# Optimization experiments

Measured on AMD Instinct MI355X. Metric: run time of the kernel, lower is better.

Reference implementation:

```python
import jax, jax.numpy as jnp
import numpy as np

EPS = 1e-12  # matches torch F.normalize clamp_min eps
SCALE = 20.0
NEG = -1e9


def l2norm(x):
    return x / jnp.maximum(jnp.linalg.norm(x, axis=-1, keepdims=True), EPS)


def setup_inputs() -> dict:
    key = jax.random.key(0)
    B, P, A, DV, DT, E = 32, 192, 30, 768, 768, 256
    ks = jax.random.split(key, 8)
    visual_feature = jax.random.normal(ks[0], (B, 1 + P, DV), jnp.float32)
    textual_feature = jax.random.normal(ks[1], (B, 1 + A, DT), jnp.float32)
    att_nums = jax.random.randint(ks[2], (B,), 1, A + 1)  # valid attr counts >=1
    # mask==1 marks padded attribute slots (consistent with att_nums)
    mask = (jnp.arange(A)[None, :] >= att_nums[:, None]).astype(jnp.int32)
    W_vis = 0.02 * jax.random.normal(ks[3], (E, DV), jnp.float32)
    W_txt = 0.02 * jax.random.normal(ks[4], (E, DT), jnp.float32)
    W_patch = 0.02 * jax.random.normal(ks[5], (E, DV), jnp.float32)
    W_att = 0.02 * jax.random.normal(ks[6], (E, DT), jnp.float32)
    z = jnp.zeros((E,), jnp.float32)
    return {
        "visual_feature": visual_feature, "textual_feature": textual_feature,
        "mask": mask, "att_nums": att_nums,
        "W_vis": W_vis, "b_vis": z, "W_txt": W_txt, "b_txt": z,
        "W_patch": W_patch, "b_patch": z, "W_att": W_att, "b_att": z,
    }


def reference(visual_feature, textual_feature, mask, att_nums,
              W_vis, b_vis, W_txt, b_txt, W_patch, b_patch, W_att, b_att):
    # token splits + linear projections
    visual_embed = visual_feature[:, 0] @ W_vis.T + b_vis        # [Bv, E]
    patch = visual_feature[:, 1:] @ W_patch.T + b_patch           # [Bv, P, E]
    textual_embed = textual_feature[:, 0] @ W_txt.T + b_txt       # [Bt, E]
    att = textual_feature[:, 1:] @ W_att.T + b_att                # [Bt, A, E]

    pad = mask.astype(bool)                                       # [Bt, A], True = padded

    # attention 1: each text's attributes attend over every image's patches
    s1 = jax.nn.relu(jnp.einsum('tae,vpe->vtap', l2norm(att), l2norm(patch))) * SCALE
    attn1 = jax.nn.softmax(s1, axis=-1)                           # [Bv, Bt, A, P]
    attend_patch = jnp.einsum('vtap,vpe->vtae', attn1, patch)     # [Bv, Bt, A, E]
    attend_patch = jnp.where(pad[None, :, :, None], 0.0, attend_patch)

    # attention 2: each image's patches attend over every text's attributes (masked)
    s2 = jax.nn.relu(jnp.einsum('vpe,tae->tvpa', l2norm(patch), l2norm(att))) * SCALE
    s2 = jnp.where(pad[:, None, None, :], NEG, s2)                # [Bt, Bv, P, A]
    attn2 = jax.nn.softmax(s2, axis=-1)
    attend_att = jnp.einsum('tvpa,tae->tvpe', attn2, att)         # [Bt, Bv, P, E]

    # local similarity
    ap = l2norm(attend_patch)                                     # [Bv, Bt, A, E]
    aa = l2norm(attend_att)                                       # [Bt, Bv, P, E]
    an = att_nums.astype(aa.dtype)
    sim = jnp.einsum('tvpe,vtae->tvpa', aa, ap) / an[:, None, None, None]
    local_similarity = sim.sum(axis=2).mean(axis=2)               # [Bt, Bv]

    # training-path global embeds
    patch_mean = patch.mean(axis=1)                               # [Bv, E]
    att_mean = (att / an[:, None, None]).sum(axis=1)              # [Bt, E]

    return (visual_embed, textual_embed, patch_mean, att_mean, local_similarity)
```

## Files before the change

kernel.cpp:

```cpp
#include <hip/hip_runtime.h>
#include <math.h>

#define D_IN 768
#define E_DIM 256
#define NB 32
#define NP 192
#define NA 30

#define A_SLOTS (452 * 24 * 64)
#define B_SLOTS (4 * 16 * 24 * 64)

typedef __attribute__((ext_vector_type(8))) __bf16 bf16x8;
typedef __attribute__((ext_vector_type(4))) float f32x4;

__device__ __forceinline__ bf16x8 cvt8(float4 a, float4 b) {
    bf16x8 v;
    v[0]=(__bf16)a.x; v[1]=(__bf16)a.y; v[2]=(__bf16)a.z; v[3]=(__bf16)a.w;
    v[4]=(__bf16)b.x; v[5]=(__bf16)b.y; v[6]=(__bf16)b.z; v[7]=(__bf16)b.w;
    return v;
}

__global__ __launch_bounds__(256) void prepack_kernel(
    const float* __restrict__ vf, const float* __restrict__ tf,
    const float* __restrict__ Wp, const float* __restrict__ Wa,
    const float* __restrict__ Wv, const float* __restrict__ Wt,
    __bf16* __restrict__ Apack, __bf16* __restrict__ Bpack)
{
    const int s = blockIdx.x * 256 + threadIdx.x;
    if (s < A_SLOTS) {
        const int r16 = s / 1536;
        const int rem = s - r16 * 1536;
        const int kt = rem >> 6, l = rem & 63;
        const int row16 = l & 15;
        const int k0 = kt * 32 + (l >> 4) * 8;
        const float* src;
        if (r16 < 384) {
            const int v = r16 / 12, sub = r16 - 12 * v;
            src = vf + (size_t)(v * 193 + 1 + sub * 16 + row16) * D_IN;
        } else if (r16 < 448) {
            const int u = r16 - 384, t = u >> 1, half = u & 1;
            const int ridx = half * 16 + row16;
            const int r = (ridx < NA) ? ridx : 0;
            src = tf + (size_t)(t * 31 + 1 + r) * D_IN;
        } else if (r16 < 450) {
            src = vf + (size_t)((r16 - 448) * 16 + row16) * 193 * D_IN;
        } else {
            src = tf + (size_t)((r16 - 450) * 16 + row16) * 31 * D_IN;
        }
        float4 f0 = *(const float4*)&src[k0];
        float4 f1 = *(const float4*)&src[k0 + 4];
        *(bf16x8*)&Apack[(size_t)s * 8] = cvt8(f0, f1);
    } else {
        const int u = s - A_SLOTS;
        const int mat = u / 24576;
        const int rem = u - mat * 24576;
        const int ntile = rem / 1536;
        const int rem2 = rem - ntile * 1536;
        const int kt = rem2 >> 6, l = rem2 & 63;
        const float* W;
        if (mat == 0)      W = Wp;
        else if (mat == 1) W = Wa;
        else if (mat == 2) W = Wv;
        else               W = Wt;
        const int k0 = kt * 32 + (l >> 4) * 8;
        const float* src = W + (size_t)(ntile * 16 + (l & 15)) * D_IN;
        float4 f0 = *(const float4*)&src[k0];
        float4 f1 = *(const float4*)&src[k0 + 4];
        *(bf16x8*)&Bpack[(size_t)u * 8] = cvt8(f0, f1);
    }
}

__global__ __launch_bounds__(256) void gemm_frag_kernel(
    const __bf16* __restrict__ Apack, const __bf16* __restrict__ Bpack,
    __bf16* __restrict__ Ybf)
{
    const int bid = blockIdx.x;
    const int r16 = bid >> 2, cg = bid & 3;
    const int tid = threadIdx.x;
    const int w = tid >> 6, l = tid & 63, q = l >> 4, n15 = l & 15;
    const int ntg = cg * 4 + w;
    const int mat = (r16 < 384) ? 0 : (r16 < 448) ? 1 : (r16 < 450) ? 2 : 3;

    const __bf16* Ab = Apack + (size_t)r16 * 24 * 512 + l * 8;
    const __bf16* Bb = Bpack + (size_t)(mat * 16 + ntg) * 24 * 512 + l * 8;

    f32x4 acc = {0.f, 0.f, 0.f, 0.f};
    #pragma unroll 8
    for (int kt = 0; kt < 24; ++kt) {
        bf16x8 a = *(const bf16x8*)&Ab[kt * 512];
        bf16x8 b = *(const bf16x8*)&Bb[kt * 512];
        acc = __builtin_amdgcn_mfma_f32_16x16x32_bf16(a, b, acc, 0, 0, 0);
    }

    const int col = ntg * 16 + n15;
    #pragma unroll
    for (int r = 0; r < 4; ++r)
        Ybf[(size_t)(r16 * 16 + q * 4 + r) * E_DIM + col] = (__bf16)acc[r];
}

__global__ __launch_bounds__(256) void pack_kernel(
    const __bf16* __restrict__ Ybf,
    const float* __restrict__ bv, const float* __restrict__ bt,
    const float* __restrict__ bp, const float* __restrict__ ba,
    const int* __restrict__ att_nums,
    float* __restrict__ out_vis, float* __restrict__ out_txt,
    float* __restrict__ out_pm, float* __restrict__ out_am,
    __bf16* __restrict__ pn_frag, __bf16* __restrict__ pB_frag,
    __bf16* __restrict__ an_frag, __bf16* __restrict__ attT_frag)
{
    __shared__ float LDSf[32 * 260];
    __shared__ float invn_s[32];

    const int bid = blockIdx.x;
    const int tid = threadIdx.x;

    int role, base;
    const float* bias;
    if (bid < 192)       { role = 0; base = 32 * bid;              bias = bp; }
    else if (bid < 224)  { role = 1; base = 6144 + 32 * (bid-192); bias = ba; }
    else if (bid == 224) { role = 2; base = 7168;                  bias = bv; }
    else                 { role = 3; base = 7200;                  bias = bt; }

    if (role >= 2) {
        float* outp = (role == 2) ? out_vis : out_txt;
        const float b = bias[tid];
        #pragma unroll
        for (int i = 0; i < 32; ++i)
            outp[i * E_DIM + tid] = (float)Ybf[(size_t)(base + i) * E_DIM + tid] + b;
        return;
    }

    {
        const float b = bias[tid];
        #pragma unroll
        for (int i = 0; i < 32; ++i)
            LDSf[i * 260 + tid] = (float)Ybf[(size_t)(base + i) * E_DIM + tid] + b;
    }
    __syncthreads();

    if (role == 0) {
        const int v = bid / 6, c = bid - 6 * v;
        {
            const int row = tid >> 3, seg = tid & 7;
            const float* rr = &LDSf[row * 260 + seg * 32];
            float ssq = 0.f;
            #pragma unroll
            for (int j = 0; j < 32; ++j) ssq += rr[j] * rr[j];
            ssq += __shfl_xor(ssq, 1, 64);
            ssq += __shfl_xor(ssq, 2, 64);
            ssq += __shfl_xor(ssq, 4, 64);
            if (seg == 0) invn_s[row] = 1.f / fmaxf(sqrtf(ssq), 1e-12f);
        }
        {
            float s = 0.f;
            #pragma unroll
            for (int r = 0; r < 32; ++r) s += LDSf[r * 260 + tid];
            atomicAdd(&out_pm[v * E_DIM + tid], s * (1.f / 192.f));
        }
        __syncthreads();
        __bf16* dstn = pn_frag + (size_t)(v * 6 + c) * 8192;
        #pragma unroll
        for (int i = 0; i < 4; ++i) {
            const int slot = tid + 256 * i;
            const int mt = slot >> 9, koct = (slot >> 6) & 7, lane = slot & 63;
            const int prl = mt * 16 + (lane & 15);
            const int e0 = koct * 32 + (lane >> 4) * 8;
            const float inr = invn_s[prl];
            const float* src = &LDSf[prl * 260 + e0];
            bf16x8 vv;
            #pragma unroll
            for (int j = 0; j < 8; ++j) vv[j] = (__bf16)(src[j] * inr);
            *(bf16x8*)&dstn[slot * 8] = vv;
        }
        __bf16* dstb = pB_frag + (size_t)(v * 6 + c) * 8192;
        #pragma unroll
        for (int i = 0; i < 4; ++i) {
            const int slot = tid + 256 * i;
            const int nt = slot >> 6, lane = slot & 63;
            const int e = nt * 16 + (lane & 15);
            const int p0 = (lane >> 4) * 8;
            bf16x8 vv;
            #pragma unroll
            for (int j = 0; j < 8; ++j) vv[j] = (__bf16)LDSf[(p0 + j) * 260 + e];
            *(bf16x8*)&dstb[slot * 8] = vv;
        }
    } else {
        const int t = bid - 192;
        const int Av = att_nums[t];
        {
            const int row = tid >> 3, seg = tid & 7;
            const float* rr = &LDSf[row * 260 + seg * 32];
            float ssq = 0.f;
            #pragma unroll
            for (int j = 0; j < 32; ++j) ssq += rr[j] * rr[j];
            ssq += __shfl_xor(ssq, 1, 64);
            ssq += __shfl_xor(ssq, 2, 64);
            ssq += __shfl_xor(ssq, 4, 64);
            if (seg == 0) invn_s[row] = (row < NA) ? 1.f / fmaxf(sqrtf(ssq), 1e-12f) : 0.f;
        }
        {
            float s = 0.f;
            #pragma unroll
            for (int r = 0; r < NA; ++r) s += LDSf[r * 260 + tid];
            out_am[t * E_DIM + tid] = s / (float)Av;
        }
        __syncthreads();
        __bf16* dstn = an_frag + (size_t)t * 8192;
        #pragma unroll
        for (int i = 0; i < 4; ++i) {
            const int slot = tid + 256 * i;
            const int at = slot >> 9, koct = (slot >> 6) & 7, lane = slot & 63;
            const int a = at * 16 + (lane & 15);
            const int e0 = koct * 32 + (lane >> 4) * 8;
            const float inr = (a < NA) ? invn_s[a] : 0.f;
            const float* src = &LDSf[a * 260 + e0];
            bf16x8 vv;
            #pragma unroll
            for (int j = 0; j < 8; ++j) vv[j] = (__bf16)(src[j] * inr);
            *(bf16x8*)&dstn[slot * 8] = vv;
        }
        __bf16* dstb = attT_frag + (size_t)t * 8192;
        #pragma unroll
        for (int i = 0; i < 4; ++i) {
            const int slot = tid + 256 * i;
            const int nt = slot >> 6, lane = slot & 63;
            const int e = nt * 16 + (lane & 15);
            const int a0 = (lane >> 4) * 8;
            bf16x8 vv;
            #pragma unroll
            for (int j = 0; j < 8; ++j)
                vv[j] = (a0 + j < NA) ? (__bf16)LDSf[(a0 + j) * 260 + e] : (__bf16)0.f;
            *(bf16x8*)&dstb[slot * 8] = vv;
        }
    }
}

__global__ __launch_bounds__(256) void pair_mfma_kernel(
    const __bf16* __restrict__ pn_frag, const __bf16* __restrict__ pB_frag,
    const __bf16* __restrict__ an_frag, const __bf16* __restrict__ attT_frag,
    const int* __restrict__ att_nums, float* __restrict__ out_sim)
{
    __shared__ __align__(16) __bf16 an_s[8192];
    __shared__ __align__(16) __bf16 attT_s[8192];
    __shared__ __align__(16) __bf16 pn_s[8192];
    __shared__ __align__(16) __bf16 pB_s[8192];
    __shared__ __align__(16) __bf16 Xa_s[1024];
    __shared__ __align__(16) __bf16 XaT_s[1024];
    __shared__ float red_s[128];
    __shared__ float invn_s[32];
    __shared__ float wred_s[4];

    const int v = blockIdx.x, t = blockIdx.y;
    const int tid = threadIdx.x;
    const int w = tid >> 6, l = tid & 63, q = l >> 4, n15 = l & 15;
    const int Av = att_nums[t];

    {
        const __bf16* s1 = an_frag + (size_t)t * 8192;
        const __bf16* s2 = attT_frag + (size_t)t * 8192;
        #pragma unroll
        for (int i = 0; i < 4; ++i) {
            const int slot = tid + 256 * i;
            *(bf16x8*)&an_s[slot * 8]   = *(const bf16x8*)&s1[slot * 8];
            *(bf16x8*)&attT_s[slot * 8] = *(const bf16x8*)&s2[slot * 8];
        }
    }
    __syncthreads();

    bf16x8 ab[4];
    #pragma unroll
    for (int n = 0; n < 4; ++n)
        ab[n] = *(const bf16x8*)&attT_s[((w * 4 + n) * 64 + l) * 8];

    f32x4 apacc[2][4];
    #pragma unroll
    for (int m = 0; m < 2; ++m)
        #pragma unroll
        for (int n = 0; n < 4; ++n) { f32x4 z = {0.f,0.f,0.f,0.f}; apacc[m][n] = z; }
    float sa_acc[4] = {0.f, 0.f, 0.f, 0.f};

    for (int c = 0; c < 6; ++c) {
        __syncthreads();
        {
            const __bf16* sp1 = pn_frag + (size_t)(v * 6 + c) * 8192;
            const __bf16* sp2 = pB_frag + (size_t)(v * 6 + c) * 8192;
            #pragma unroll
            for (int i = 0; i < 4; ++i) {
                const int slot = tid + 256 * i;
                *(bf16x8*)&pn_s[slot * 8] = *(const bf16x8*)&sp1[slot * 8];
                *(bf16x8*)&pB_s[slot * 8] = *(const bf16x8*)&sp2[slot * 8];
            }
        }
        __syncthreads();

        {
            const int mt = w >> 1, at = w & 1;
            f32x4 sacc = {0.f, 0.f, 0.f, 0.f};
            #pragma unroll
            for (int kp = 0; kp < 8; ++kp) {
                bf16x8 af  = *(const bf16x8*)&pn_s[((mt * 8 + kp) * 64 + l) * 8];
                bf16x8 bf_ = *(const bf16x8*)&an_s[((at * 8 + kp) * 64 + l) * 8];
                sacc = __builtin_amdgcn_mfma_f32_16x16x32_bf16(af, bf_, sacc, 0, 0, 0);
            }
            const int a = at * 16 + n15;
            #pragma unroll
            for (int r = 0; r < 4; ++r) {
                const int pcl = q * 4 + r;
                const int pcc = mt * 16 + pcl;
                float xvv = (a < Av) ? __expf(fmaxf(20.f * sacc[r], 0.f)) : 0.f;
                __bf16 h = (__bf16)xvv;
                Xa_s[mt * 512 + (pcl + 16 * (a >> 3)) * 8 + (a & 7)] = h;
                XaT_s[at * 512 + (n15 + 16 * (pcc >> 3)) * 8 + (pcc & 7)] = h;
            }
        }
        __syncthreads();

        f32x4 aacc[2][4];
        {
            bf16x8 xa0 = *(const bf16x8*)&Xa_s[l * 8];
            bf16x8 xa1 = *(const bf16x8*)&Xa_s[512 + l * 8];
            bf16x8 xt0 = *(const bf16x8*)&XaT_s[l * 8];
            bf16x8 xt1 = *(const bf16x8*)&XaT_s[512 + l * 8];
            #pragma unroll
            for (int n = 0; n < 4; ++n) {
                f32x4 z = {0.f, 0.f, 0.f, 0.f};
                aacc[0][n] = __builtin_amdgcn_mfma_f32_16x16x32_bf16(xa0, ab[n], z, 0, 0, 0);
                aacc[1][n] = __builtin_amdgcn_mfma_f32_16x16x32_bf16(xa1, ab[n], z, 0, 0, 0);
                bf16x8 pb = *(const bf16x8*)&pB_s[((w * 4 + n) * 64 + l) * 8];
                apacc[0][n] = __builtin_amdgcn_mfma_f32_16x16x32_bf16(xt0, pb, apacc[0][n], 0, 0, 0);
                apacc[1][n] = __builtin_amdgcn_mfma_f32_16x16x32_bf16(xt1, pb, apacc[1][n], 0, 0, 0);
            }
        }

        #pragma unroll
        for (int mt2 = 0; mt2 < 2; ++mt2)
            #pragma unroll
            for (int r = 0; r < 4; ++r) {
                float ssq = 0.f;
                #pragma unroll
                for (int n = 0; n < 4; ++n) { float vv = aacc[mt2][n][r]; ssq += vv * vv; }
                ssq += __shfl_xor(ssq, 1, 64);
                ssq += __shfl_xor(ssq, 2, 64);
                ssq += __shfl_xor(ssq, 4, 64);
                ssq += __shfl_xor(ssq, 8, 64);
                if (n15 == 0) red_s[(mt2 * 16 + q * 4 + r) * 4 + w] = ssq;
            }
        __syncthreads();
        if (tid < 32) {
            float s = red_s[tid * 4] + red_s[tid * 4 + 1] + red_s[tid * 4 + 2] + red_s[tid * 4 + 3];
            invn_s[tid] = 1.f / fmaxf(sqrtf(s), 1e-12f);
        }
        __syncthreads();
        #pragma unroll
        for (int mt2 = 0; mt2 < 2; ++mt2)
            #pragma unroll
            for (int r = 0; r < 4; ++r) {
                const float inr = invn_s[mt2 * 16 + q * 4 + r];
                #pragma unroll
                for (int n = 0; n < 4; ++n) sa_acc[n] += aacc[mt2][n][r] * inr;
            }
    }

    #pragma unroll
    for (int mt2 = 0; mt2 < 2; ++mt2)
        #pragma unroll
        for (int r = 0; r < 4; ++r) {
            float ssq = 0.f;
            #pragma unroll
            for (int n = 0; n < 4; ++n) { float vv = apacc[mt2][n][r]; ssq += vv * vv; }
            ssq += __shfl_xor(ssq, 1, 64);
            ssq += __shfl_xor(ssq, 2, 64);
            ssq += __shfl_xor(ssq, 4, 64);
            ssq += __shfl_xor(ssq, 8, 64);
            if (n15 == 0) red_s[(mt2 * 16 + q * 4 + r) * 4 + w] = ssq;
        }
    __syncthreads();
    if (tid < 32) {
        float s = red_s[tid * 4] + red_s[tid * 4 + 1] + red_s[tid * 4 + 2] + red_s[tid * 4 + 3];
        invn_s[tid] = 1.f / fmaxf(sqrtf(s), 1e-12f);
    }
    __syncthreads();

    float prod = 0.f;
    #pragma unroll
    for (int n = 0; n < 4; ++n) {
        float sp = 0.f;
        #pragma unroll
        for (int mt2 = 0; mt2 < 2; ++mt2)
            #pragma unroll
            for (int r = 0; r < 4; ++r)
                sp += apacc[mt2][n][r] * invn_s[mt2 * 16 + q * 4 + r];
        float saf = sa_acc[n];
        saf += __shfl_xor(saf, 16, 64);
        saf += __shfl_xor(saf, 32, 64);
        float spf = sp;
        spf += __shfl_xor(spf, 16, 64);
        spf += __shfl_xor(spf, 32, 64);
        prod += saf * spf;
    }
    prod += __shfl_xor(prod, 1, 64);
    prod += __shfl_xor(prod, 2, 64);
    prod += __shfl_xor(prod, 4, 64);
    prod += __shfl_xor(prod, 8, 64);
    prod += __shfl_xor(prod, 16, 64);
    prod += __shfl_xor(prod, 32, 64);
    if (l == 0) wred_s[w] = prod;
    __syncthreads();
    if (tid == 0)
        out_sim[t * NB + v] = (wred_s[0] + wred_s[1] + wred_s[2] + wred_s[3]) * 0.25f
                              / ((float)Av * 30.f);
}

extern "C" void kernel_launch(void* const* d_in, const int* in_sizes, int n_in,
                              void* d_out, int out_size, void* d_ws, size_t ws_size,
                              hipStream_t stream)
{
    const float* vf = (const float*)d_in[0];
    const float* tf = (const float*)d_in[1];
    const int*   an = (const int*)d_in[3];
    const float* Wv = (const float*)d_in[4];
    const float* bv = (const float*)d_in[5];
    const float* Wt = (const float*)d_in[6];
    const float* bt = (const float*)d_in[7];
    const float* Wp = (const float*)d_in[8];
    const float* bp = (const float*)d_in[9];
    const float* Wa = (const float*)d_in[10];
    const float* ba = (const float*)d_in[11];

    float* out = (float*)d_out;
    float* out_vis = out;
    float* out_txt = out + 8192;
    float* out_pm  = out + 16384;
    float* out_am  = out + 24576;
    float* out_sim = out + 32768;

    __bf16* Ybf = (__bf16*)d_ws;
    char* region2 = (char*)d_ws + 3702784;
    __bf16* Apack = (__bf16*)region2;
    __bf16* Bpack = Apack + (size_t)A_SLOTS * 8;
    __bf16* pn_frag   = (__bf16*)region2;
    __bf16* pB_frag   = pn_frag + 1572864;
    __bf16* an_frag   = pn_frag + 3145728;
    __bf16* attT_frag = pn_frag + 3407872;

    hipMemsetAsync((char*)d_out + 16384 * sizeof(float), 0, 8192 * sizeof(float), stream);

    prepack_kernel<<<(A_SLOTS + B_SLOTS) / 256, 256, 0, stream>>>(
        vf, tf, Wp, Wa, Wv, Wt, Apack, Bpack);

    gemm_frag_kernel<<<452 * 4, 256, 0, stream>>>(Apack, Bpack, Ybf);

    pack_kernel<<<226, 256, 0, stream>>>(
        Ybf, bv, bt, bp, ba, an,
        out_vis, out_txt, out_pm, out_am,
        pn_frag, pB_frag, an_frag, attT_frag);

    pair_mfma_kernel<<<dim3(NB, NB), 256, 0, stream>>>(
        pn_frag, pB_frag, an_frag, attT_frag, an, out_sim);
}
```

Before: 154.7 us.

## Fuse projection GEMM with fragment packing and stream pair-kernel operands from global

Merges the projection GEMM and the pack/normalize kernel into one kernel where each block computes a 16-row strip across all 256 columns, keeping results in LDS instead of round-tripping through a bf16 Ybf buffer. The output-zeroing memset is folded into the prepack kernel, and att_mean now accumulates via atomics from two half-blocks. In the pair kernel, patch and attribute fragments are read directly from global into registers rather than staged through LDS, and the norm reduction is recomputed per lane to remove barriers. This cuts launches, intermediate traffic and LDS usage, but the fused GEMM has fewer blocks (452) and the pair kernel now depends on cache hits for repeated global fragment loads.

```diff
diff --git a/kernel.cpp b/kernel.cpp
--- a/kernel.cpp
+++ b/kernel.cpp
@@ -24,9 +24,11 @@
     const float* __restrict__ vf, const float* __restrict__ tf,
     const float* __restrict__ Wp, const float* __restrict__ Wa,
     const float* __restrict__ Wv, const float* __restrict__ Wt,
-    __bf16* __restrict__ Apack, __bf16* __restrict__ Bpack)
+    __bf16* __restrict__ Apack, __bf16* __restrict__ Bpack,
+    float* __restrict__ out_zero)
 {
     const int s = blockIdx.x * 256 + threadIdx.x;
+    if (s < 16384) out_zero[s] = 0.f;
     if (s < A_SLOTS) {
         const int r16 = s / 1536;
         const int rem = s - r16 * 1536;
@@ -70,36 +72,8 @@
     }
 }
 
-__global__ __launch_bounds__(256) void gemm_frag_kernel(
+__global__ __launch_bounds__(256) void gemm_pack_kernel(
     const __bf16* __restrict__ Apack, const __bf16* __restrict__ Bpack,
-    __bf16* __restrict__ Ybf)
-{
-    const int bid = blockIdx.x;
-    const int r16 = bid >> 2, cg = bid & 3;
-    const int tid = threadIdx.x;
-    const int w = tid >> 6, l = tid & 63, q = l >> 4, n15 = l & 15;
-    const int ntg = cg * 4 + w;
-    const int mat = (r16 < 384) ? 0 : (r16 < 448) ? 1 : (r16 < 450) ? 2 : 3;
-
-    const __bf16* Ab = Apack + (size_t)r16 * 24 * 512 + l * 8;
-    const __bf16* Bb = Bpack + (size_t)(mat * 16 + ntg) * 24 * 512 + l * 8;
-
-    f32x4 acc = {0.f, 0.f, 0.f, 0.f};
-    #pragma unroll 8
-    for (int kt = 0; kt < 24; ++kt) {
-        bf16x8 a = *(const bf16x8*)&Ab[kt * 512];
-        bf16x8 b = *(const bf16x8*)&Bb[kt * 512];
-        acc = __builtin_amdgcn_mfma_f32_16x16x32_bf16(a, b, acc, 0, 0, 0);
-    }
-
-    const int col = ntg * 16 + n15;
-    #pragma unroll
-    for (int r = 0; r < 4; ++r)
-        Ybf[(size_t)(r16 * 16 + q * 4 + r) * E_DIM + col] = (__bf16)acc[r];
-}
-
-__global__ __launch_bounds__(256) void pack_kernel(
-    const __bf16* __restrict__ Ybf,
     const float* __restrict__ bv, const float* __restrict__ bt,
     const float* __restrict__ bp, const float* __restrict__ ba,
     const int* __restrict__ att_nums,
@@ -108,169 +82,152 @@
     __bf16* __restrict__ pn_frag, __bf16* __restrict__ pB_frag,
     __bf16* __restrict__ an_frag, __bf16* __restrict__ attT_frag)
 {
-    __shared__ float LDSf[32 * 260];
-    __shared__ float invn_s[32];
-
-    const int bid = blockIdx.x;
+    __shared__ float LDSf[16 * 260];
+    __shared__ float invn_s[16];
+
+    const int r16 = blockIdx.x;
     const int tid = threadIdx.x;
-
-    int role, base;
-    const float* bias;
-    if (bid < 192)       { role = 0; base = 32 * bid;              bias = bp; }
-    else if (bid < 224)  { role = 1; base = 6144 + 32 * (bid-192); bias = ba; }
-    else if (bid == 224) { role = 2; base = 7168;                  bias = bv; }
-    else                 { role = 3; base = 7200;                  bias = bt; }
-
-    if (role >= 2) {
-        float* outp = (role == 2) ? out_vis : out_txt;
-        const float b = bias[tid];
-        #pragma unroll
-        for (int i = 0; i < 32; ++i)
-            outp[i * E_DIM + tid] = (float)Ybf[(size_t)(base + i) * E_DIM + tid] + b;
+    const int w = tid >> 6, l = tid & 63, q = l >> 4, n15 = l & 15;
+    const int mat = (r16 < 384) ? 0 : (r16 < 448) ? 1 : (r16 < 450) ? 2 : 3;
+    const float* bias = (mat == 0) ? bp : (mat == 1) ? ba : (mat == 2) ? bv : bt;
+
+    const __bf16* Ab = Apack + (size_t)r16 * 24 * 512 + l * 8;
+    const __bf16* Bb = Bpack + ((size_t)(mat * 16 + w * 4) * 24 * 512) + l * 8;
+
+    f32x4 acc[4];
+    #pragma unroll
+    for (int n = 0; n < 4; ++n) { f32x4 z = {0.f,0.f,0.f,0.f}; acc[n] = z; }
+
+    #pragma unroll 6
+    for (int kt = 0; kt < 24; ++kt) {
+        bf16x8 a = *(const bf16x8*)&Ab[kt * 512];
+        #pragma unroll
+        for (int nt = 0; nt < 4; ++nt) {
+            bf16x8 b = *(const bf16x8*)&Bb[(size_t)nt * 24 * 512 + kt * 512];
+            acc[nt] = __builtin_amdgcn_mfma_f32_16x16x32_bf16(a, b, acc[nt], 0, 0, 0);
+        }
+    }
+
+    #pragma unroll
+    for (int nt = 0; nt < 4; ++nt) {
+        const int col = w * 64 + nt * 16 + n15;
+        const float b = bias[col];
+        #pragma unroll
+        for (int r = 0; r < 4; ++r)
+            LDSf[(q * 4 + r) * 260 + col] = acc[nt][r] + b;
+    }
+    __syncthreads();
+
+    if (mat >= 2) {
+        float* outp = (mat == 2) ? out_vis : out_txt;
+        const int rowbase = (mat == 2) ? (r16 - 448) * 16 : (r16 - 450) * 16;
+        #pragma unroll
+        for (int i = 0; i < 16; ++i)
+            outp[(rowbase + i) * E_DIM + tid] = LDSf[i * 260 + tid];
         return;
     }
 
+    const bool is_patch = (mat == 0);
+    int vc = 0, mt = 0, t = 0, Av = 1;
+    if (is_patch) {
+        const int v = r16 / 12, sub = r16 - 12 * v;
+        vc = v * 6 + (sub >> 1);  mt = sub & 1;
+    } else {
+        const int u = r16 - 384;
+        t = u >> 1;  mt = u & 1;  Av = att_nums[t];
+    }
+
     {
-        const float b = bias[tid];
-        #pragma unroll
-        for (int i = 0; i < 32; ++i)
-            LDSf[i * 260 + tid] = (float)Ybf[(size_t)(base + i) * E_DIM + tid] + b;
-    }
-    __syncthreads();
-
-    if (role == 0) {
-        const int v = bid / 6, c = bid - 6 * v;
-        {
-            const int row = tid >> 3, seg = tid & 7;
-            const float* rr = &LDSf[row * 260 + seg * 32];
-            float ssq = 0.f;
-            #pragma unroll
-            for (int j = 0; j < 32; ++j) ssq += rr[j] * rr[j];
-            ssq += __shfl_xor(ssq, 1, 64);
-            ssq += __shfl_xor(ssq, 2, 64);
-            ssq += __shfl_xor(ssq, 4, 64);
-            if (seg == 0) invn_s[row] = 1.f / fmaxf(sqrtf(ssq), 1e-12f);
-        }
-        {
-            float s = 0.f;
-            #pragma unroll
-            for (int r = 0; r < 32; ++r) s += LDSf[r * 260 + tid];
-            atomicAdd(&out_pm[v * E_DIM + tid], s * (1.f / 192.f));
-        }
-        __syncthreads();
-        __bf16* dstn = pn_frag + (size_t)(v * 6 + c) * 8192;
-        #pragma unroll
-        for (int i = 0; i < 4; ++i) {
-            const int slot = tid + 256 * i;
-            const int mt = slot >> 9, koct = (slot >> 6) & 7, lane = slot & 63;
-            const int prl = mt * 16 + (lane & 15);
+        const int row = tid >> 4, seg = tid & 15;
+        const float* rr = &LDSf[row * 260 + seg * 16];
+        float ssq = 0.f;
+        #pragma unroll
+        for (int j = 0; j < 16; ++j) ssq += rr[j] * rr[j];
+        ssq += __shfl_xor(ssq, 1, 64);
+        ssq += __shfl_xor(ssq, 2, 64);
+        ssq += __shfl_xor(ssq, 4, 64);
+        ssq += __shfl_xor(ssq, 8, 64);
+        if (seg == 0) {
+            const bool valid = is_patch || (mt * 16 + row < NA);
+            invn_s[row] = valid ? 1.f / fmaxf(sqrtf(ssq), 1e-12f) : 0.f;
+        }
+    }
+    {
+        const int nrows = is_patch ? 16 : (mt == 0 ? 16 : 14);
+        float s = 0.f;
+        for (int r = 0; r < nrows; ++r) s += LDSf[r * 260 + tid];
+        if (is_patch) atomicAdd(&out_pm[(r16 / 12) * E_DIM + tid], s * (1.f / 192.f));
+        else          atomicAdd(&out_am[t * E_DIM + tid], s / (float)Av);
+    }
+    __syncthreads();
+
+    {
+        __bf16* dstn = (is_patch ? pn_frag + (size_t)vc * 8192
+                                 : an_frag + (size_t)t * 8192) + (size_t)mt * 4096;
+        #pragma unroll
+        for (int ii = 0; ii < 2; ++ii) {
+            const int s2 = tid + 256 * ii;
+            const int koct = s2 >> 6, lane = s2 & 63;
+            const int rloc = lane & 15;
             const int e0 = koct * 32 + (lane >> 4) * 8;
-            const float inr = invn_s[prl];
-            const float* src = &LDSf[prl * 260 + e0];
+            const float inr = invn_s[rloc];
+            const float* src = &LDSf[rloc * 260 + e0];
             bf16x8 vv;
             #pragma unroll
             for (int j = 0; j < 8; ++j) vv[j] = (__bf16)(src[j] * inr);
-            *(bf16x8*)&dstn[slot * 8] = vv;
-        }
-        __bf16* dstb = pB_frag + (size_t)(v * 6 + c) * 8192;
-        #pragma unroll
-        for (int i = 0; i < 4; ++i) {
-            const int slot = tid + 256 * i;
-            const int nt = slot >> 6, lane = slot & 63;
-            const int e = nt * 16 + (lane & 15);
-            const int p0 = (lane >> 4) * 8;
+            *(bf16x8*)&dstn[(size_t)s2 * 8] = vv;
+        }
+    }
+    {
+        __bf16* dstb = is_patch ? pB_frag + (size_t)vc * 8192
+                                : attT_frag + (size_t)t * 8192;
+        #pragma unroll
+        for (int ii = 0; ii < 2; ++ii) {
+            const int s2 = tid + 256 * ii;
+            const int nt = s2 >> 5, li = s2 & 31;
+            const int lane = 32 * mt + li;
+            const int p0 = (li >> 4) * 8;
+            const int e = nt * 16 + (li & 15);
             bf16x8 vv;
             #pragma unroll
-            for (int j = 0; j < 8; ++j) vv[j] = (__bf16)LDSf[(p0 + j) * 260 + e];
-            *(bf16x8*)&dstb[slot * 8] = vv;
-        }
-    } else {
-        const int t = bid - 192;
-        const int Av = att_nums[t];
-        {
-            const int row = tid >> 3, seg = tid & 7;
-            const float* rr = &LDSf[row * 260 + seg * 32];
-            float ssq = 0.f;
-            #pragma unroll
-            for (int j = 0; j < 32; ++j) ssq += rr[j] * rr[j];
-            ssq += __shfl_xor(ssq, 1, 64);
-            ssq += __shfl_xor(ssq, 2, 64);
-            ssq += __shfl_xor(ssq, 4, 64);
-            if (seg == 0) invn_s[row] = (row < NA) ? 1.f / fmaxf(sqrtf(ssq), 1e-12f) : 0.f;
-        }
-        {
-            float s = 0.f;
-            #pragma unroll
-            for (int r = 0; r < NA; ++r) s += LDSf[r * 260 + tid];
-            out_am[t * E_DIM + tid] = s / (float)Av;
-        }
-        __syncthreads();
-        __bf16* dstn = an_frag + (size_t)t * 8192;
-        #pragma unroll
-        for (int i = 0; i < 4; ++i) {
-            const int slot = tid + 256 * i;
-            const int at = slot >> 9, koct = (slot >> 6) & 7, lane = slot & 63;
-            const int a = at * 16 + (lane & 15);
-            const int e0 = koct * 32 + (lane >> 4) * 8;
-            const float inr = (a < NA) ? invn_s[a] : 0.f;
-            const float* src = &LDSf[a * 260 + e0];
-            bf16x8 vv;
-            #pragma unroll
-            for (int j = 0; j < 8; ++j) vv[j] = (__bf16)(src[j] * inr);
-            *(bf16x8*)&dstn[slot * 8] = vv;
-        }
-        __bf16* dstb = attT_frag + (size_t)t * 8192;
-        #pragma unroll
-        for (int i = 0; i < 4; ++i) {
-            const int slot = tid + 256 * i;
-            const int nt = slot >> 6, lane = slot & 63;
-            const int e = nt * 16 + (lane & 15);
-            const int a0 = (lane >> 4) * 8;
-            bf16x8 vv;
-            #pragma unroll
-            for (int j = 0; j < 8; ++j)
-                vv[j] = (a0 + j < NA) ? (__bf16)LDSf[(a0 + j) * 260 + e] : (__bf16)0.f;
-            *(bf16x8*)&dstb[slot * 8] = vv;
+            for (int j = 0; j < 8; ++j) {
+                float val = LDSf[(p0 + j) * 260 + e];
+                if (!is_patch && (mt * 16 + p0 + j >= NA)) val = 0.f;
+                vv[j] = (__bf16)val;
+            }
+            *(bf16x8*)&dstb[(size_t)(nt * 64 + lane) * 8] = vv;
         }
     }
 }
 
-__global__ __launch_bounds__(256) void pair_mfma_kernel(
+__global__ __launch_bounds__(256, 3) void pair_mfma_kernel(
     const __bf16* __restrict__ pn_frag, const __bf16* __restrict__ pB_frag,
     const __bf16* __restrict__ an_frag, const __bf16* __restrict__ attT_frag,
     const int* __restrict__ att_nums, float* __restrict__ out_sim)
 {
     __shared__ __align__(16) __bf16 an_s[8192];
-    __shared__ __align__(16) __bf16 attT_s[8192];
-    __shared__ __align__(16) __bf16 pn_s[8192];
-    __shared__ __align__(16) __bf16 pB_s[8192];
     __shared__ __align__(16) __bf16 Xa_s[1024];
     __shared__ __align__(16) __bf16 XaT_s[1024];
     __shared__ float red_s[128];
-    __shared__ float invn_s[32];
     __shared__ float wred_s[4];
 
     const int v = blockIdx.x, t = blockIdx.y;
     const int tid = threadIdx.x;
     const int w = tid >> 6, l = tid & 63, q = l >> 4, n15 = l & 15;
     const int Av = att_nums[t];
+    const int mt = w >> 1, at = w & 1;
 
     {
         const __bf16* s1 = an_frag + (size_t)t * 8192;
-        const __bf16* s2 = attT_frag + (size_t)t * 8192;
         #pragma unroll
         for (int i = 0; i < 4; ++i) {
             const int slot = tid + 256 * i;
-            *(bf16x8*)&an_s[slot * 8]   = *(const bf16x8*)&s1[slot * 8];
-            *(bf16x8*)&attT_s[slot * 8] = *(const bf16x8*)&s2[slot * 8];
-        }
-    }
-    __syncthreads();
-
-    bf16x8 ab[4];
-    #pragma unroll
-    for (int n = 0; n < 4; ++n)
-        ab[n] = *(const bf16x8*)&attT_s[((w * 4 + n) * 64 + l) * 8];
+            *(bf16x8*)&an_s[slot * 8] = *(const bf16x8*)&s1[slot * 8];
+        }
+    }
+    __syncthreads();
+
+    const __bf16* atb = attT_frag + (size_t)t * 8192;
 
     f32x4 apacc[2][4];
     #pragma unroll
@@ -280,25 +237,21 @@
     float sa_acc[4] = {0.f, 0.f, 0.f, 0.f};
 
     for (int c = 0; c < 6; ++c) {
-        __syncthreads();
+        const __bf16* pnb = pn_frag + (size_t)(v * 6 + c) * 8192;
+        const __bf16* pbb = pB_frag + (size_t)(v * 6 + c) * 8192;
+
+        bf16x8 pb[4], ab[4];
+        #pragma unroll
+        for (int n = 0; n < 4; ++n) {
+            pb[n] = *(const bf16x8*)&pbb[((w * 4 + n) * 64 + l) * 8];
+            ab[n] = *(const bf16x8*)&atb[((w * 4 + n) * 64 + l) * 8];
+        }
+
         {
-            const __bf16* sp1 = pn_frag + (size_t)(v * 6 + c) * 8192;
-            const __bf16* sp2 = pB_frag + (size_t)(v * 6 + c) * 8192;
-            #pragma unroll
-            for (int i = 0; i < 4; ++i) {
-                const int slot = tid + 256 * i;
-                *(bf16x8*)&pn_s[slot * 8] = *(const bf16x8*)&sp1[slot * 8];
-                *(bf16x8*)&pB_s[slot * 8] = *(const bf16x8*)&sp2[slot * 8];
-            }
-        }
-        __syncthreads();
-
-        {
-            const int mt = w >> 1, at = w & 1;
             f32x4 sacc = {0.f, 0.f, 0.f, 0.f};
             #pragma unroll
             for (int kp = 0; kp < 8; ++kp) {
-                bf16x8 af  = *(const bf16x8*)&pn_s[((mt * 8 + kp) * 64 + l) * 8];
+                bf16x8 af  = *(const bf16x8*)&pnb[((mt * 8 + kp) * 64 + l) * 8];
                 bf16x8 bf_ = *(const bf16x8*)&an_s[((at * 8 + kp) * 64 + l) * 8];
                 sacc = __builtin_amdgcn_mfma_f32_16x16x32_bf16(af, bf_, sacc, 0, 0, 0);
             }
@@ -326,12 +279,10 @@
                 f32x4 z = {0.f, 0.f, 0.f, 0.f};
                 aacc[0][n] = __builtin_amdgcn_mfma_f32_16x16x32_bf16(xa0, ab[n], z, 0, 0, 0);
                 aacc[1][n] = __builtin_amdgcn_mfma_f32_16x16x32_bf16(xa1, ab[n], z, 0, 0, 0);
-                bf16x8 pb = *(const bf16x8*)&pB_s[((w * 4 + n) * 64 + l) * 8];
-                apacc[0][n] = __builtin_amdgcn_mfma_f32_16x16x32_bf16(xt0, pb, apacc[0][n], 0, 0, 0);
-                apacc[1][n] = __builtin_amdgcn_mfma_f32_16x16x32_bf16(xt1, pb, apacc[1][n], 0, 0, 0);
-            }
-        }
-
+                apacc[0][n] = __builtin_amdgcn_mfma_f32_16x16x32_bf16(xt0, pb[n], apacc[0][n], 0, 0, 0);
+                apacc[1][n] = __builtin_amdgcn_mfma_f32_16x16x32_bf16(xt1, pb[n], apacc[1][n], 0, 0, 0);
+            }
+        }
         #pragma unroll
         for (int mt2 = 0; mt2 < 2; ++mt2)
             #pragma unroll
@@ -346,21 +297,20 @@
                 if (n15 == 0) red_s[(mt2 * 16 + q * 4 + r) * 4 + w] = ssq;
             }
         __syncthreads();
-        if (tid < 32) {
-            float s = red_s[tid * 4] + red_s[tid * 4 + 1] + red_s[tid * 4 + 2] + red_s[tid * 4 + 3];
-            invn_s[tid] = 1.f / fmaxf(sqrtf(s), 1e-12f);
-        }
-        __syncthreads();
         #pragma unroll
         for (int mt2 = 0; mt2 < 2; ++mt2)
             #pragma unroll
             for (int r = 0; r < 4; ++r) {
-                const float inr = invn_s[mt2 * 16 + q * 4 + r];
+                const int row = mt2 * 16 + q * 4 + r;
+                const float s = red_s[row * 4] + red_s[row * 4 + 1]
+                              + red_s[row * 4 + 2] + red_s[row * 4 + 3];
+                const float inr = 1.f / fmaxf(sqrtf(s), 1e-12f);
                 #pragma unroll
                 for (int n = 0; n < 4; ++n) sa_acc[n] += aacc[mt2][n][r] * inr;
             }
     }
 
+    __syncthreads();
     #pragma unroll
     for (int mt2 = 0; mt2 < 2; ++mt2)
         #pragma unroll
@@ -375,11 +325,17 @@
             if (n15 == 0) red_s[(mt2 * 16 + q * 4 + r) * 4 + w] = ssq;
         }
     __syncthreads();
-    if (tid < 32) {
-        float s = red_s[tid * 4] + red_s[tid * 4 + 1] + red_s[tid * 4 + 2] + red_s[tid * 4 + 3];
-        invn_s[tid] = 1.f / fmaxf(sqrtf(s), 1e-12f);
-    }
-    __syncthreads();
+
+    float inr_ap[2][4];
+    #pragma unroll
+    for (int mt2 = 0; mt2 < 2; ++mt2)
+        #pragma unroll
+        for (int r = 0; r < 4; ++r) {
+            const int row = mt2 * 16 + q * 4 + r;
+            const float s = red_s[row * 4] + red_s[row * 4 + 1]
+                          + red_s[row * 4 + 2] + red_s[row * 4 + 3];
+            inr_ap[mt2][r] = 1.f / fmaxf(sqrtf(s), 1e-12f);
+        }
 
     float prod = 0.f;
     #pragma unroll
@@ -389,7 +345,7 @@
         for (int mt2 = 0; mt2 < 2; ++mt2)
             #pragma unroll
             for (int r = 0; r < 4; ++r)
-                sp += apacc[mt2][n][r] * invn_s[mt2 * 16 + q * 4 + r];
+                sp += apacc[mt2][n][r] * inr_ap[mt2][r];
         float saf = sa_acc[n];
         saf += __shfl_xor(saf, 16, 64);
         saf += __shfl_xor(saf, 32, 64);
@@ -434,24 +390,19 @@
     float* out_am  = out + 24576;
     float* out_sim = out + 32768;
 
-    __bf16* Ybf = (__bf16*)d_ws;
-    char* region2 = (char*)d_ws + 3702784;
-    __bf16* Apack = (__bf16*)region2;
+    __bf16* Apack = (__bf16*)d_ws;
     __bf16* Bpack = Apack + (size_t)A_SLOTS * 8;
-    __bf16* pn_frag   = (__bf16*)region2;
-    __bf16* pB_frag   = pn_frag + 1572864;
-    __bf16* an_frag   = pn_frag + 3145728;
-    __bf16* attT_frag = pn_frag + 3407872;
-
-    hipMemsetAsync((char*)d_out + 16384 * sizeof(float), 0, 8192 * sizeof(float), stream);
+    __bf16* frag0 = Bpack + (size_t)B_SLOTS * 8;
+    __bf16* pn_frag   = frag0;
+    __bf16* pB_frag   = frag0 + 1572864;
+    __bf16* an_frag   = frag0 + 3145728;
+    __bf16* attT_frag = frag0 + 3407872;
 
     prepack_kernel<<<(A_SLOTS + B_SLOTS) / 256, 256, 0, stream>>>(
-        vf, tf, Wp, Wa, Wv, Wt, Apack, Bpack);
-
-    gemm_frag_kernel<<<452 * 4, 256, 0, stream>>>(Apack, Bpack, Ybf);
-
-    pack_kernel<<<226, 256, 0, stream>>>(
-        Ybf, bv, bt, bp, ba, an,
+        vf, tf, Wp, Wa, Wv, Wt, Apack, Bpack, out + 16384);
+
+    gemm_pack_kernel<<<452, 256, 0, stream>>>(
+        Apack, Bpack, bv, bt, bp, ba, an,
         out_vis, out_txt, out_pm, out_am,
         pn_frag, pB_frag, an_frag, attT_frag);
 
```

Result: faster. 149.6 us (-3.3%).
